# Optimization experiments

Measured on AMD Instinct MI355X. Metric: run time of the kernel, lower is better.

Reference implementation:

```python
import jax, jax.numpy as jnp
import numpy as np

# ---- constants from init_kwargs ----
LAM = 0.05      # lam_l2
CG_MAX = 10     # cg_max
B, C, H, W = 8, 12, 384, 384
EPS = 1e-12


def _cplx(a):
    # [..., 2] real/imag -> complex
    return jax.lax.complex(a[..., 0], a[..., 1])


def _ri(z):
    return jnp.stack([jnp.real(z), jnp.imag(z)], axis=-1)


def setup_inputs() -> dict:
    key = jax.random.key(0)
    k1, k2, k3, k4 = jax.random.split(key, 4)
    x = jax.random.normal(k1, (B, H, W, 2), dtype=jnp.float32)
    adj = jax.random.normal(k2, (B, H, W, 2), dtype=jnp.float32)  # A^H b
    maps = jax.random.normal(k3, (B, C, H, W, 2), dtype=jnp.float32) / np.sqrt(C).astype(np.float32)
    mask = (jax.random.uniform(k4, (B, H, W)) < 0.4).astype(jnp.float32)
    return {"x": x, "adj": adj, "maps": maps, "mask": mask}


def reference(x, adj, maps, mask):
    xc = _cplx(x)          # [B,H,W] complex image (network estimate)
    adjc = _cplx(adj)      # [B,H,W] A^H b
    mc = _cplx(maps)       # [B,C,H,W] coil sensitivities
    maskc = mask.astype(jnp.complex64)[:, None]  # [B,1,H,W]

    def normal(v):
        # SENSE normal operator: A^H A v
        cim = mc * v[:, None]                               # [B,C,H,W]
        k = jnp.fft.fft2(cim, norm="ortho")
        im = jnp.fft.ifft2(k * maskc, norm="ortho")
        return jnp.sum(jnp.conj(mc) * im, axis=1)           # [B,H,W]

    def Aop(v):
        # (A^H A + lam I) v
        return normal(v) + LAM * v

    def zdot(a, b):
        # per-batch real inner product Re<a,b>
        return jnp.real(jnp.sum(jnp.conj(a) * b, axis=(1, 2)))[:, None, None]

    # rhs = adj + lam * x ; CG initialized at rhs (flare.ConjGrad.forward(rhs))
    rhs = adjc + LAM * xc
    x0 = rhs
    r = rhs - Aop(x0)
    p = r
    rd = zdot(r, r)

    def step(carry, _):
        xk, r, p, rd = carry
        Ap = Aop(p)
        alpha = rd / (zdot(p, Ap) + EPS)
        xk = xk + alpha * p
        r = r - alpha * Ap
        rd_new = zdot(r, r)
        beta = rd_new / (rd + EPS)
        p = r + beta * p
        return (xk, r, p, rd_new), None

    (xk, _, _, _), _ = jax.lax.scan(step, (x0, r, p, rd), None, length=CG_MAX)
    return _ri(xk)  # [B,H,W,2]
```

## Files before the change

kernel.cpp:

```cpp
#include <hip/hip_runtime.h>
#include <math.h>

#define BB 8
#define CC 12
#define HH 384
#define WW 384
#define NPIX (HH*WW)
#define LAMF 0.05f
#define EPSF 1e-12f
#define NITER 10

typedef float2 c2;

__device__ __forceinline__ c2 mkc(float x, float y){ c2 r; r.x=x; r.y=y; return r; }
__device__ __forceinline__ c2 cadd(c2 a, c2 b){ return mkc(a.x+b.x, a.y+b.y); }
__device__ __forceinline__ c2 csub(c2 a, c2 b){ return mkc(a.x-b.x, a.y-b.y); }
__device__ __forceinline__ c2 cmul(c2 a, c2 b){ return mkc(a.x*b.x - a.y*b.y, a.x*b.y + a.y*b.x); }
__device__ __forceinline__ c2 cmulcj(c2 a, c2 b){ return mkc(a.x*b.x + a.y*b.y, a.x*b.y - a.y*b.x); }
__device__ __forceinline__ c2 cax(float s, c2 a, c2 b){ return mkc(fmaf(s,a.x,b.x), fmaf(s,a.y,b.y)); }
__device__ __forceinline__ c2 rot90(c2 a, float d){ return mkc(d*a.y, -d*a.x); }

__device__ __forceinline__ void lds_fence(){
  asm volatile("s_waitcnt lgkmcnt(0)" ::: "memory");
}
__device__ __forceinline__ void cbar(){
  asm volatile("" ::: "memory");
}

template<int DIR> __device__ __forceinline__ void dft3(c2&a0,c2&a1,c2&a2){
  const float d=(float)DIR;
  c2 t=cadd(a1,a2), s=csub(a1,a2);
  c2 m=mkc(a0.x-0.5f*t.x, a0.y-0.5f*t.y);
  const float c=0.8660254037844386f*d;
  c2 w=mkc(c*s.y, -c*s.x);
  a0=cadd(a0,t); a1=cadd(m,w); a2=csub(m,w);
}
template<int DIR> __device__ __forceinline__ void dft6(c2 u[6]){
  c2 e0=u[0],e1=u[2],e2=u[4], o0=u[1],o1=u[3],o2=u[5];
  dft3<DIR>(e0,e1,e2); dft3<DIR>(o0,o1,o2);
  const float d=(float)DIR, q=0.8660254037844386f*d;
  c2 w1=mkc(0.5f,-q), w2=mkc(-0.5f,-q);
  c2 b1=cmul(w1,o1), b2=cmul(w2,o2);
  u[0]=cadd(e0,o0); u[3]=csub(e0,o0);
  u[1]=cadd(e1,b1); u[4]=csub(e1,b1);
  u[2]=cadd(e2,b2); u[5]=csub(e2,b2);
}
template<int DIR> __device__ __forceinline__ void dft8(c2 u[8]){
  const float d=(float)DIR;
  c2 t0=cadd(u[0],u[4]), t1=csub(u[0],u[4]);
  c2 t2=cadd(u[2],u[6]), t3=csub(u[2],u[6]);
  c2 E0=cadd(t0,t2), E2=csub(t0,t2);
  c2 r3=rot90(t3,d);
  c2 E1=cadd(t1,r3), E3=csub(t1,r3);
  c2 s0=cadd(u[1],u[5]), s1=csub(u[1],u[5]);
  c2 s2=cadd(u[3],u[7]), s3=csub(u[3],u[7]);
  c2 O0=cadd(s0,s2), O2v=csub(s0,s2);
  c2 r7=rot90(s3,d);
  c2 O1=cadd(s1,r7), O3=csub(s1,r7);
  const float rs=0.7071067811865476f;
  c2 w81=mkc(rs,-rs*d), w83=mkc(-rs,-rs*d);
  O1=cmul(w81,O1); O2v=rot90(O2v,d); O3=cmul(w83,O3);
  u[0]=cadd(E0,O0); u[4]=csub(E0,O0);
  u[1]=cadd(E1,O1); u[5]=csub(E1,O1);
  u[2]=cadd(E2,O2v); u[6]=csub(E2,O2v);
  u[3]=cadd(E3,O3); u[7]=csub(E3,O3);
}

__device__ __forceinline__ int pidx(int i){ return i + (i/48); }

__device__ __forceinline__ c2 twid(float rev){
  float r = rev - floorf(rev);
  return mkc(__builtin_amdgcn_cosf(r), -__builtin_amdgcn_sinf(r));
}

__device__ __forceinline__ void make_tw(int t, c2 tw2[7], c2 tw3[7]){
  int k2 = t % 6;
  #pragma unroll
  for (int j=1;j<8;j++){
    tw2[j-1] = twid((float)(k2*j) * (1.0f/48.0f));
    tw3[j-1] = twid((float)(t*j)  * (1.0f/384.0f));
  }
}

template<int DIR>
__device__ __forceinline__ void fft384(c2 u6[6], c2 o8[8], c2* S,
                                       int t, const c2 tw2[7], const c2 tw3[7])
{
  dft6<DIR>(u6);
  cbar();
  #pragma unroll
  for (int j=0;j<6;j++) S[pidx(6*t+j)] = u6[j];
  lds_fence();
  if (t<48){
    c2 u[8];
    #pragma unroll
    for (int j=0;j<8;j++) u[j]=S[pidx(t+48*j)];
    #pragma unroll
    for (int j=1;j<8;j++){
      c2 w=tw2[j-1]; if (DIR<0) w.y=-w.y;
      u[j]=cmul(u[j],w);
    }
    dft8<DIR>(u);
    int k=t%6; int base=(t-k)*8+k;
    cbar();
    #pragma unroll
    for (int j=0;j<8;j++) S[pidx(base+6*j)]=u[j];
    lds_fence();
    c2 v[8];
    #pragma unroll
    for (int j=0;j<8;j++) v[j]=S[pidx(t+48*j)];
    #pragma unroll
    for (int j=1;j<8;j++){
      c2 w=tw3[j-1]; if (DIR<0) w.y=-w.y;
      v[j]=cmul(v[j],w);
    }
    dft8<DIR>(v);
    #pragma unroll
    for (int j=0;j<8;j++) o8[j]=v[j];
  }
  cbar();
}

template<int MODE>
__global__ __launch_bounds__(256)
void k1_fwd(const c2* __restrict__ xin, const c2* __restrict__ adj,
            const c2* __restrict__ maps, c2* __restrict__ WK,
            const c2* __restrict__ rbuf, const c2* __restrict__ pin,
            c2* __restrict__ pout, const float* __restrict__ bNum,
            const float* __restrict__ bDen)
{
  __shared__ c2 tile[8][387];
  __shared__ c2 scratch[4][392];
  const int tid=threadIdx.x, t=tid&63, wv=tid>>6;
  const int NT=HH/8;
  int bid=blockIdx.x;
  int ht=bid%NT, c=(bid/NT)%CC, b=bid/(NT*CC);
  int h0=ht*8;
  c2 tw2[7], tw3[7]; make_tw(t,tw2,tw3);
  float beta=0.f;
  if (MODE==1) beta = bNum[b]/(bDen[b]+EPSF);
  c2* S=scratch[wv];
  const c2* mb = maps + (size_t)(b*CC+c)*NPIX;
  for (int i=0;i<2;i++){
    int rr=wv*2+i, h=h0+rr;
    size_t ro=((size_t)b*HH+h)*WW;
    const c2* mrow=mb+(size_t)h*WW;
    c2 u6[6];
    #pragma unroll
    for (int j=0;j<6;j++){
      int w=t+64*j;
      c2 v;
      if (MODE==0){
        v = cax(LAMF, xin[ro+w], adj[ro+w]);
      } else {
        v = cax(beta, pin[ro+w], rbuf[ro+w]);
        if (c==0) pout[ro+w]=v;
      }
      u6[j]=cmul(mrow[w], v);
    }
    c2 o8[8];
    fft384<1>(u6,o8,S,t,tw2,tw3);
    if (t<48){
      #pragma unroll
      for (int j=0;j<8;j++) tile[rr][t+48*j]=o8[j];
    }
  }
  __syncthreads();
  c2* wkc = WK + (size_t)(b*CC+c)*NPIX;
  int rl=tid&7, wg=tid>>3;
  for (int it=0;it<12;it++){
    int w=it*32+wg;
    wkc[(size_t)w*HH + h0 + rl] = tile[rl][w];
  }
}

__global__ __launch_bounds__(256)
void k2_mid(c2* __restrict__ WK, const float* __restrict__ maskT)
{
  __shared__ c2 scratch[4][392];
  const int tid=threadIdx.x, t=tid&63, wv=tid>>6;
  const int NT=WW/16;
  int bid=blockIdx.x;
  int wt=bid%NT, c=(bid/NT)%CC, b=bid/(NT*CC);
  c2 tw2[7], tw3[7]; make_tw(t,tw2,tw3);
  c2* S=scratch[wv];
  for (int i=0;i<4;i++){
    int w=wt*16+wv*4+i;
    c2* row = WK + ((size_t)(b*CC+c)*WW + w)*HH;
    const float* mrow = maskT + ((size_t)b*WW + w)*HH;
    c2 u6[6];
    #pragma unroll
    for (int j=0;j<6;j++) u6[j]=row[t+64*j];
    c2 o8[8];
    fft384<1>(u6,o8,S,t,tw2,tw3);
    if (t<48){
      #pragma unroll
      for (int j=0;j<8;j++){
        float m=mrow[t+48*j];
        c2 v=o8[j];
        S[t+48*j]=mkc(v.x*m, v.y*m);
      }
    }
    lds_fence();
    #pragma unroll
    for (int j=0;j<6;j++) u6[j]=S[t+64*j];
    c2 o8b[8];
    fft384<-1>(u6,o8b,S,t,tw2,tw3);
    if (t<48){
      #pragma unroll
      for (int j=0;j<8;j++) row[t+48*j]=o8b[j];
    }
  }
}

template<int MODE>
__global__ __launch_bounds__(256)
void k3_inv(const c2* __restrict__ WK, const c2* __restrict__ maps,
            const c2* __restrict__ xin, const c2* __restrict__ adj,
            const c2* __restrict__ pin, c2* __restrict__ rbuf,
            c2* __restrict__ Apbuf, c2* __restrict__ xout,
            float* __restrict__ accslot)
{
  __shared__ c2 tile[8][387];
  __shared__ c2 scratch[4][392];
  const int tid=threadIdx.x, t=tid&63, wv=tid>>6;
  const int NT=HH/8;
  int bid=blockIdx.x;
  int ht=bid%NT, b=bid/NT;
  int h0=ht*8;
  c2 tw2[7],tw3[7]; make_tw(t,tw2,tw3);
  c2* S=scratch[wv];
  c2 acc[2][8];
  #pragma unroll
  for(int a=0;a<2;a++){
    #pragma unroll
    for(int q=0;q<8;q++) acc[a][q]=mkc(0.f,0.f);
  }
  int jj=tid&7, wq=tid>>3;
  for (int c=0;c<CC;c++){
    const c2* wkc = WK + (size_t)(b*CC+c)*NPIX;
    __syncthreads();
    for (int it=0;it<12;it++){
      int w=it*32+wq;
      tile[jj][w]=wkc[(size_t)w*HH + h0 + jj];
    }
    __syncthreads();
    const c2* mb = maps + (size_t)(b*CC+c)*NPIX;
    #pragma unroll
    for (int rl=0;rl<2;rl++){
      int j=wv*2+rl, h=h0+j;
      c2 u6[6];
      #pragma unroll
      for (int q=0;q<6;q++) u6[q]=tile[j][t+64*q];
      c2 o8[8];
      fft384<-1>(u6,o8,S,t,tw2,tw3);
      if (t<48){
        const c2* mrow=mb+(size_t)h*WW;
        #pragma unroll
        for (int q=0;q<8;q++){
          acc[rl][q]=cadd(acc[rl][q], cmulcj(mrow[t+48*q], o8[q]));
        }
      }
    }
  }
  float partial=0.f;
  #pragma unroll
  for (int rl=0;rl<2;rl++){
    int h=h0+wv*2+rl;
    size_t ro=((size_t)b*HH+h)*WW;
    if (t<48){
      #pragma unroll
      for (int q=0;q<8;q++){
        int w=t+48*q;
        if (MODE==0){
          c2 rhs = cax(LAMF, xin[ro+w], adj[ro+w]);
          c2 Ap = cax(LAMF, rhs, acc[rl][q]);
          c2 rv = csub(rhs, Ap);
          rbuf[ro+w]=rv;
          xout[ro+w]=rhs;
          partial = fmaf(rv.x,rv.x,fmaf(rv.y,rv.y,partial));
        } else {
          c2 pv = pin[ro+w];
          c2 Ap = cax(LAMF, pv, acc[rl][q]);
          Apbuf[ro+w]=Ap;
          partial = fmaf(pv.x,Ap.x,fmaf(pv.y,Ap.y,partial));
        }
      }
    }
  }
  #pragma unroll
  for (int o=32;o>0;o>>=1) partial += __shfl_down(partial,o);
  if (t==0) atomicAdd(&accslot[b], partial);
}

__global__ __launch_bounds__(256)
void k4_upd(c2* __restrict__ x, c2* __restrict__ rbuf,
            const c2* __restrict__ p, const c2* __restrict__ Ap,
            const float* __restrict__ rdPrev, const float* __restrict__ pApk,
            float* __restrict__ rdNew)
{
  const int PERB = NPIX/1024;
  int bid=blockIdx.x;
  int b=bid/PERB, blk=bid%PERB;
  float alpha = rdPrev[b]/(pApk[b]+EPSF);
  size_t base=(size_t)b*NPIX + (size_t)blk*1024 + threadIdx.x;
  float partial=0.f;
  #pragma unroll
  for (int i=0;i<4;i++){
    size_t idx=base + i*256;
    c2 pv=p[idx], apv=Ap[idx], xv=x[idx], rv=rbuf[idx];
    xv = cax(alpha, pv, xv);
    rv = cax(-alpha, apv, rv);
    x[idx]=xv; rbuf[idx]=rv;
    partial = fmaf(rv.x,rv.x,fmaf(rv.y,rv.y,partial));
  }
  #pragma unroll
  for (int o=32;o>0;o>>=1) partial += __shfl_down(partial,o);
  if ((threadIdx.x&63)==0) atomicAdd(&rdNew[b], partial);
}

__global__ void kzero(float* scal){ scal[threadIdx.x]=0.f; }

__global__ __launch_bounds__(256)
void kmask(const float* __restrict__ mask, float* __restrict__ maskT)
{
  __shared__ float tile[32][33];
  int bid=blockIdx.x;
  int wt=bid%12, htl=(bid/12)%12, b=bid/144;
  int h0=htl*32, w0=wt*32;
  int tid=threadIdx.x;
  int wl=tid&31, hl=tid>>5;
  for (int it=0;it<4;it++){
    int h=h0+it*8+hl;
    tile[it*8+hl][wl]=mask[((size_t)b*HH+h)*WW + w0+wl];
  }
  __syncthreads();
  int hl2=tid&31, wl2=tid>>5;
  const float SC = 1.0f/((float)HH*(float)WW);
  for (int it=0;it<4;it++){
    int w=w0+it*8+wl2;
    maskT[((size_t)b*WW+w)*HH + h0+hl2] = SC*tile[hl2][it*8+wl2];
  }
}

extern "C" void kernel_launch(void* const* d_in, const int* in_sizes, int n_in,
                              void* d_out, int out_size, void* d_ws, size_t ws_size,
                              hipStream_t stream)
{
  const c2* xin=(const c2*)d_in[0];
  const c2* adj=(const c2*)d_in[1];
  const c2* maps=(const c2*)d_in[2];
  const float* mask=(const float*)d_in[3];
  c2* xout=(c2*)d_out;
  char* wsp=(char*)d_ws;
  size_t off=0;
  c2* WK=(c2*)(wsp+off);    off += (size_t)BB*CC*NPIX*sizeof(c2);
  float* maskT=(float*)(wsp+off); off += (size_t)BB*NPIX*sizeof(float);
  c2* rbuf=(c2*)(wsp+off);  off += (size_t)BB*NPIX*sizeof(c2);
  c2* pA=(c2*)(wsp+off);    off += (size_t)BB*NPIX*sizeof(c2);
  c2* pB=(c2*)(wsp+off);    off += (size_t)BB*NPIX*sizeof(c2);
  c2* Apb=(c2*)(wsp+off);   off += (size_t)BB*NPIX*sizeof(c2);
  float* scal=(float*)(wsp+off);
  float* rd=scal;
  float* pAp=scal+11*BB;
  float* zslot=scal+22*BB;

  kzero<<<1,256,0,stream>>>(scal);
  kmask<<<BB*144,256,0,stream>>>(mask,maskT);

  k1_fwd<0><<<BB*CC*(HH/8),256,0,stream>>>(xin,adj,maps,WK,rbuf,pA,pB,zslot,zslot);
  k2_mid<<<BB*CC*(WW/16),256,0,stream>>>(WK,maskT);
  k3_inv<0><<<BB*(HH/8),256,0,stream>>>(WK,maps,xin,adj,pA,rbuf,Apb,xout,rd);

  for (int k=1;k<=NITER;k++){
    c2* pouT = (k&1)? pA: pB;
    c2* pinb = (k&1)? pB: pA;
    const float* bN = (k>=2)? rd+(size_t)(k-1)*BB : zslot;
    const float* bD = (k>=2)? rd+(size_t)(k-2)*BB : zslot;
    k1_fwd<1><<<BB*CC*(HH/8),256,0,stream>>>(xin,adj,maps,WK,rbuf,pinb,pouT,bN,bD);
    k2_mid<<<BB*CC*(WW/16),256,0,stream>>>(WK,maskT);
    k3_inv<1><<<BB*(HH/8),256,0,stream>>>(WK,maps,xin,adj,pouT,rbuf,Apb,xout,pAp+(size_t)k*BB);
    k4_upd<<<BB*(NPIX/1024),256,0,stream>>>(xout,rbuf,pouT,Apb,rd+(size_t)(k-1)*BB,pAp+(size_t)k*BB,rd+(size_t)k*BB);
  }
}
```

Baseline: 3.422 ms.

## Halve k3 row tile and register-prefetch next coil's k-space tile

Result: faster. 3.217 ms (-6.0%).

```diff
diff --git a/kernel.cpp b/kernel.cpp
--- a/kernel.cpp
+++ b/kernel.cpp
@@ -221,70 +221,80 @@
             c2* __restrict__ Apbuf, c2* __restrict__ xout,
             float* __restrict__ accslot)
 {
-  __shared__ c2 tile[8][387];
+  __shared__ c2 tile[4][387];
   __shared__ c2 scratch[4][392];
   const int tid=threadIdx.x, t=tid&63, wv=tid>>6;
-  const int NT=HH/8;
+  const int NT=HH/4;
   int bid=blockIdx.x;
   int ht=bid%NT, b=bid/NT;
-  int h0=ht*8;
+  int h0=ht*4;
   c2 tw2[7],tw3[7]; make_tw(t,tw2,tw3);
   c2* S=scratch[wv];
-  c2 acc[2][8];
-  #pragma unroll
-  for(int a=0;a<2;a++){
-    #pragma unroll
-    for(int q=0;q<8;q++) acc[a][q]=mkc(0.f,0.f);
-  }
-  int jj=tid&7, wq=tid>>3;
+  const int h=h0+wv;
+  const c2* mrow0 = maps + ((size_t)(b*CC)*HH + h)*WW;
+  c2 acc[8];
+  #pragma unroll
+  for(int q=0;q<8;q++) acc[q]=mkc(0.f,0.f);
+
+  c2 pre[6];
+  {
+    const c2* wkc = WK + (size_t)(b*CC)*NPIX;
+    #pragma unroll
+    for (int it=0; it<6; ++it){
+      int e = it*256 + tid;
+      pre[it] = wkc[(size_t)(e>>2)*HH + h0 + (e&3)];
+    }
+  }
   for (int c=0;c<CC;c++){
-    const c2* wkc = WK + (size_t)(b*CC+c)*NPIX;
     __syncthreads();
-    for (int it=0;it<12;it++){
-      int w=it*32+wq;
-      tile[jj][w]=wkc[(size_t)w*HH + h0 + jj];
+    #pragma unroll
+    for (int it=0; it<6; ++it){
+      int e = it*256 + tid;
+      tile[e&3][e>>2] = pre[it];
+    }
+    if (c+1<CC){
+      const c2* wkc = WK + (size_t)(b*CC+c+1)*NPIX;
+      #pragma unroll
+      for (int it=0; it<6; ++it){
+        int e = it*256 + tid;
+        pre[it] = wkc[(size_t)(e>>2)*HH + h0 + (e&3)];
+      }
+    }
+    c2 mreg[8];
+    if (t<48){
+      const c2* mrow = mrow0 + (size_t)c*NPIX;
+      #pragma unroll
+      for (int q=0;q<8;q++) mreg[q]=mrow[t+48*q];
     }
     __syncthreads();
-    const c2* mb = maps + (size_t)(b*CC+c)*NPIX;
-    #pragma unroll
-    for (int rl=0;rl<2;rl++){
-      int j=wv*2+rl, h=h0+j;
-      c2 u6[6];
-      #pragma unroll
-      for (int q=0;q<6;q++) u6[q]=tile[j][t+64*q];
-      c2 o8[8];
-      fft384<-1>(u6,o8,S,t,tw2,tw3);
-      if (t<48){
-        const c2* mrow=mb+(size_t)h*WW;
-        #pragma unroll
-        for (int q=0;q<8;q++){
-          acc[rl][q]=cadd(acc[rl][q], cmulcj(mrow[t+48*q], o8[q]));
-        }
-      }
+    c2 u6[6];
+    #pragma unroll
+    for (int q=0;q<6;q++) u6[q]=tile[wv][t+64*q];
+    c2 o8[8];
+    fft384<-1>(u6,o8,S,t,tw2,tw3);
+    if (t<48){
+      #pragma unroll
+      for (int q=0;q<8;q++) acc[q]=cadd(acc[q], cmulcj(mreg[q], o8[q]));
     }
   }
   float partial=0.f;
-  #pragma unroll
-  for (int rl=0;rl<2;rl++){
-    int h=h0+wv*2+rl;
-    size_t ro=((size_t)b*HH+h)*WW;
-    if (t<48){
-      #pragma unroll
-      for (int q=0;q<8;q++){
-        int w=t+48*q;
-        if (MODE==0){
-          c2 rhs = cax(LAMF, xin[ro+w], adj[ro+w]);
-          c2 Ap = cax(LAMF, rhs, acc[rl][q]);
-          c2 rv = csub(rhs, Ap);
-          rbuf[ro+w]=rv;
-          xout[ro+w]=rhs;
-          partial = fmaf(rv.x,rv.x,fmaf(rv.y,rv.y,partial));
-        } else {
-          c2 pv = pin[ro+w];
-          c2 Ap = cax(LAMF, pv, acc[rl][q]);
-          Apbuf[ro+w]=Ap;
-          partial = fmaf(pv.x,Ap.x,fmaf(pv.y,Ap.y,partial));
-        }
+  size_t ro=((size_t)b*HH+h)*WW;
+  if (t<48){
+    #pragma unroll
+    for (int q=0;q<8;q++){
+      int w=t+48*q;
+      if (MODE==0){
+        c2 rhs = cax(LAMF, xin[ro+w], adj[ro+w]);
+        c2 Ap = cax(LAMF, rhs, acc[q]);
+        c2 rv = csub(rhs, Ap);
+        rbuf[ro+w]=rv;
+        xout[ro+w]=rhs;
+        partial = fmaf(rv.x,rv.x,fmaf(rv.y,rv.y,partial));
+      } else {
+        c2 pv = pin[ro+w];
+        c2 Ap = cax(LAMF, pv, acc[q]);
+        Apbuf[ro+w]=Ap;
+        partial = fmaf(pv.x,Ap.x,fmaf(pv.y,Ap.y,partial));
       }
     }
   }
@@ -370,7 +380,7 @@
 
   k1_fwd<0><<<BB*CC*(HH/8),256,0,stream>>>(xin,adj,maps,WK,rbuf,pA,pB,zslot,zslot);
   k2_mid<<<BB*CC*(WW/16),256,0,stream>>>(WK,maskT);
-  k3_inv<0><<<BB*(HH/8),256,0,stream>>>(WK,maps,xin,adj,pA,rbuf,Apb,xout,rd);
+  k3_inv<0><<<BB*(HH/4),256,0,stream>>>(WK,maps,xin,adj,pA,rbuf,Apb,xout,rd);
 
   for (int k=1;k<=NITER;k++){
     c2* pouT = (k&1)? pA: pB;
@@ -379,7 +389,7 @@
     const float* bD = (k>=2)? rd+(size_t)(k-2)*BB : zslot;
     k1_fwd<1><<<BB*CC*(HH/8),256,0,stream>>>(xin,adj,maps,WK,rbuf,pinb,pouT,bN,bD);
     k2_mid<<<BB*CC*(WW/16),256,0,stream>>>(WK,maskT);
-    k3_inv<1><<<BB*(HH/8),256,0,stream>>>(WK,maps,xin,adj,pouT,rbuf,Apb,xout,pAp+(size_t)k*BB);
+    k3_inv<1><<<BB*(HH/4),256,0,stream>>>(WK,maps,xin,adj,pouT,rbuf,Apb,xout,pAp+(size_t)k*BB);
     k4_upd<<<BB*(NPIX/1024),256,0,stream>>>(xout,rbuf,pouT,Apb,rd+(size_t)(k-1)*BB,pAp+(size_t)k*BB,rd+(size_t)k*BB);
   }
 }
```
